# Performance work log

Hardware: AMD Instinct MI355X
Metric: run time of the kernel (lower is better)

Reference implementation:

```python
import jax, jax.numpy as jnp
import numpy as np
import math

N = 1024
C = 128
H = 4
HD = C // H  # 32
HID = C // 2  # geom_mlp hidden


def setup_inputs() -> dict:
    key = jax.random.key(0)
    ks = jax.random.split(key, 12)
    s = 0.02
    return {
        "x": jax.random.normal(ks[0], (N, C), jnp.float32),
        "y": jax.random.normal(ks[1], (N, C), jnp.float32),
        "pos": jax.random.normal(ks[2], (N, 3), jnp.float32),
        "Wq": jax.random.normal(ks[3], (C, C), jnp.float32) * s,
        "bq": jnp.zeros((C,), jnp.float32),
        "Wk": jax.random.normal(ks[4], (C, C), jnp.float32) * s,
        "bk": jnp.zeros((C,), jnp.float32),
        "Wv": jax.random.normal(ks[5], (C, C), jnp.float32) * s,
        "bv": jnp.zeros((C,), jnp.float32),
        "W1": jax.random.normal(ks[6], (3, HID), jnp.float32) * s,
        "b1": jnp.zeros((HID,), jnp.float32),
        "W2": jax.random.normal(ks[7], (HID, C), jnp.float32) * s,
        "b2": jnp.zeros((C,), jnp.float32),
    }


def _safe_norm(sq):
    # sqrt with zero (sub)gradient at 0, matching torch.norm behavior
    pos_mask = sq > 0
    return jnp.where(pos_mask, jnp.sqrt(jnp.where(pos_mask, sq, 1.0)), 0.0)


def reference(x, y, pos, Wq, bq, Wk, bk, Wv, bv, W1, b1, W2, b2):
    # pairwise geometry
    pos_diff = pos[:, None, :] - pos[None, :, :]          # [N, N, 3]
    dist = _safe_norm(jnp.sum(pos_diff * pos_diff, -1))   # [N, N]
    geom = jax.nn.relu(pos_diff @ W1 + b1) @ W2 + b2      # [N, N, C]
    geom = geom.reshape(N, N, H, HD)                      # per-head split

    q = (x @ Wq + bq).reshape(N, H, HD)
    k = (y @ Wk + bk).reshape(N, H, HD)
    v = (y @ Wv + bv).reshape(N, H, HD)

    attn = jnp.einsum("ihd,jhd->hij", q, k) / math.sqrt(HD)  # [H, N, N]
    geom_attn = jnp.einsum("ihd,ijhd->hij", q, geom)         # [H, N, N]
    scores = attn + geom_attn - dist[None, :, :]
    p = jax.nn.softmax(scores, axis=-1)
    out = jnp.einsum("hij,jhd->ihd", p, v).reshape(N, C)     # [N, C]
    return out
```

## Files before the change

### kernel.cpp

```cpp
#include <hip/hip_runtime.h>
#include <math.h>


static __device__ __forceinline__ float dot4(float4 a, float4 b) {
  return a.x*b.x + a.y*b.y + a.z*b.z + a.w*b.w;
}

__global__ __launch_bounds__(384) void k_pre(
    const float* __restrict__ x, const float* __restrict__ y, const float* __restrict__ pos,
    const float* __restrict__ Wq, const float* __restrict__ bq,
    const float* __restrict__ Wk, const float* __restrict__ bk,
    const float* __restrict__ Wv, const float* __restrict__ bv,
    const float* __restrict__ W1, const float* __restrict__ b1,
    const float* __restrict__ W2, const float* __restrict__ b2,
    float* __restrict__ q, float* __restrict__ v,
    float* __restrict__ kT4f, float* __restrict__ uT4f,
    float* __restrict__ sA, float* __restrict__ pos4w)
{
  __shared__ float xs[256], ys[256], qs[256];
  __shared__ __align__(16) float4 W2S[64*33];

  const int t  = threadIdx.x;
  const int n0 = blockIdx.x * 2;

  if (t < 256) { xs[t] = x[n0*128 + t]; ys[t] = y[n0*128 + t]; }
  {
    const float4* w2g = (const float4*)W2;
    #pragma unroll
    for (int r = 0; r < 6; ++r) {
      const int e = t + 384*r;
      if (e < 2048) W2S[(e>>5)*33 + (e&31)] = w2g[e];
    }
  }
  __syncthreads();

  {
    const int c   = t & 127;
    const int mat = t >> 7;
    const float* W    = (mat == 0) ? Wq : (mat == 1 ? Wk : Wv);
    const float* S    = (mat == 0) ? xs : ys;
    const float* bias = (mat == 0) ? bq : (mat == 1 ? bk : bv);
    float a0 = 0.f, a1 = 0.f;
    #pragma unroll 8
    for (int d = 0; d < 128; ++d) {
      const float w_ = W[d*128 + c];
      a0 = fmaf(S[d],       w_, a0);
      a1 = fmaf(S[128 + d], w_, a1);
    }
    const float bb = bias[c];
    a0 += bb; a1 += bb;
    if (mat == 0) {
      q[n0*128 + c] = a0; q[(n0+1)*128 + c] = a1;
      qs[c] = a0; qs[128 + c] = a1;
    } else if (mat == 2) {
      v[n0*128 + c] = a0; v[(n0+1)*128 + c] = a1;
    } else {
      kT4f[((c>>2)*1024 + n0  )*4 + (c&3)] = a0;
      kT4f[((c>>2)*1024 + n0+1)*4 + (c&3)] = a1;
    }
  }
  __syncthreads();

  if (t < 256) {
    const int m = t & 63, h = t >> 6;
    const float4* qs4 = (const float4*)qs;
    #pragma unroll
    for (int ii = 0; ii < 2; ++ii) {
      float acc = 0.f;
      #pragma unroll
      for (int ch = 0; ch < 8; ++ch)
        acc += dot4(qs4[ii*32 + h*8 + ch], W2S[m*33 + h*8 + ch]);
      sA[(n0+ii)*328 + 8 + (m>>2)*20 + h*4 + (m&3)] = acc;
    }
    if (t < 8) {
      const int ii = t >> 2, h2 = t & 3;
      float ca = 0.f;
      #pragma unroll
      for (int d = 0; d < 32; ++d) ca = fmaf(qs[ii*128 + h2*32 + d], b2[h2*32 + d], ca);
      sA[(n0+ii)*328 + h2] = ca;
    } else if (t < 16) {
      const int tt = t-8, ii = tt>>2, cc = tt&3;
      sA[(n0+ii)*328 + 4 + cc] = (cc < 3) ? pos[(n0+ii)*3 + cc] : 0.f;
    } else if (t < 24) {
      const int tt = t-16, ii = tt>>2, cc = tt&3;
      pos4w[(n0+ii)*4 + cc] = (cc < 3) ? pos[(n0+ii)*3 + cc] : 0.f;
    }
  } else {
    const int tt = t - 256, ii = tt >> 6, m = tt & 63;
    float ua = 0.f;
    #pragma unroll
    for (int cc = 0; cc < 3; ++cc) ua = fmaf(pos[(n0+ii)*3 + cc], W1[cc*64 + m], ua);
    uT4f[((m>>2)*1024 + (n0+ii))*4 + (m&3)] = ua;
    sA[(n0+ii)*328 + 8 + (m>>2)*20 + 16 + (m&3)] = ua + b1[m];
  }
}

__global__ __launch_bounds__(512, 2) void k_attn(
    const float* __restrict__ q, const float* __restrict__ v,
    const float4* __restrict__ kT4, const float4* __restrict__ uT4,
    const float* __restrict__ sA, const float4* __restrict__ pos4,
    float* __restrict__ out)
{
  __shared__ __align__(16) float eL[8*512];
  __shared__ __align__(16) float rnum[2048];
  __shared__ float rden[64];

  const int t    = threadIdx.x;
  const int i0   = blockIdx.x * 2;
  const int w    = t >> 6;
  const int lane = t & 63;
  const int hl   = lane >> 4;

  const float* sA0 = sA + i0*328;
  const float* sA1 = sA0 + 328;
  const float* q0  = q + i0*128;
  const float* q1  = q0 + 128;

  const float c00 = sA0[0], c01 = sA0[1], c02 = sA0[2], c03 = sA0[3];
  const float c10 = sA1[0], c11 = sA1[1], c12 = sA1[2], c13 = sA1[3];
  const float p0x = sA0[4], p0y = sA0[5], p0z = sA0[6];
  const float p1x = sA1[4], p1y = sA1[5], p1z = sA1[6];

  float2 acc0 = make_float2(0.f, 0.f);
  float2 acc1 = make_float2(0.f, 0.f);
  float lsum[8] = {0.f,0.f,0.f,0.f,0.f,0.f,0.f,0.f};
  const float RS = 0.17677669529663687f;

  float* eW = &eL[w*512];
  const float4* er0 = (const float4*)&eL[w*512 +        hl*64];
  const float4* er1 = (const float4*)&eL[w*512 + 256 + hl*64];

  #pragma unroll
  for (int tt2 = 0; tt2 < 2; ++tt2) {
    const int jb = (w*2 + tt2) * 64;
    const int j  = jb + lane;

    const float4 pj = pos4[j];
    const float d0x = p0x-pj.x, d0y = p0y-pj.y, d0z = p0z-pj.z;
    const float d1x = p1x-pj.x, d1y = p1y-pj.y, d1z = p1z-pj.z;
    const float dist0 = sqrtf(d0x*d0x + d0y*d0y + d0z*d0z);
    const float dist1 = sqrtf(d1x*d1x + d1y*d1y + d1z*d1z);

    float g[2][4] = {{c00,c01,c02,c03},{c10,c11,c12,c13}};
    #pragma unroll 4
    for (int mb = 0; mb < 16; ++mb) {
      const float4 uj = uT4[mb*1024 + j];
      #pragma unroll
      for (int ii = 0; ii < 2; ++ii) {
        const float* ab = (ii ? sA1 : sA0) + 8 + mb*20;
        const float h0 = fmaxf(ab[16] - uj.x, 0.f);
        const float h1 = fmaxf(ab[17] - uj.y, 0.f);
        const float h2 = fmaxf(ab[18] - uj.z, 0.f);
        const float h3 = fmaxf(ab[19] - uj.w, 0.f);
        #pragma unroll
        for (int h = 0; h < 4; ++h)
          g[ii][h] += h0*ab[h*4+0] + h1*ab[h*4+1] + h2*ab[h*4+2] + h3*ab[h*4+3];
      }
    }

    float s[2][4] = {{0.f,0.f,0.f,0.f},{0.f,0.f,0.f,0.f}};
    #pragma unroll 8
    for (int cb = 0; cb < 32; ++cb) {
      const float4 kj = kT4[cb*1024 + j];
      const int h = cb >> 3;
      s[0][h] += kj.x*q0[cb*4+0] + kj.y*q0[cb*4+1] + kj.z*q0[cb*4+2] + kj.w*q0[cb*4+3];
      s[1][h] += kj.x*q1[cb*4+0] + kj.y*q1[cb*4+1] + kj.z*q1[cb*4+2] + kj.w*q1[cb*4+3];
    }

    #pragma unroll
    for (int ii = 0; ii < 2; ++ii) {
      const float di = ii ? dist1 : dist0;
      #pragma unroll
      for (int h = 0; h < 4; ++h) {
        const float p = __expf(fmaf(s[ii][h], RS, g[ii][h]) - di);
        lsum[ii*4+h] += p;
        eW[(ii*4+h)*64 + lane] = p;
      }
    }
    __builtin_amdgcn_wave_barrier();

    const float2* v2 = (const float2*)(v + jb*128);
    #pragma unroll 4
    for (int j4 = 0; j4 < 16; ++j4) {
      const float4 e0 = er0[j4];
      const float4 e1 = er1[j4];
      const float2 va = v2[(j4*4+0)*64 + lane];
      const float2 vb = v2[(j4*4+1)*64 + lane];
      const float2 vc = v2[(j4*4+2)*64 + lane];
      const float2 vd = v2[(j4*4+3)*64 + lane];
      acc0.x = fmaf(e0.x, va.x, acc0.x); acc0.y = fmaf(e0.x, va.y, acc0.y);
      acc1.x = fmaf(e1.x, va.x, acc1.x); acc1.y = fmaf(e1.x, va.y, acc1.y);
      acc0.x = fmaf(e0.y, vb.x, acc0.x); acc0.y = fmaf(e0.y, vb.y, acc0.y);
      acc1.x = fmaf(e1.y, vb.x, acc1.x); acc1.y = fmaf(e1.y, vb.y, acc1.y);
      acc0.x = fmaf(e0.z, vc.x, acc0.x); acc0.y = fmaf(e0.z, vc.y, acc0.y);
      acc1.x = fmaf(e1.z, vc.x, acc1.x); acc1.y = fmaf(e1.z, vc.y, acc1.y);
      acc0.x = fmaf(e0.w, vd.x, acc0.x); acc0.y = fmaf(e0.w, vd.y, acc0.y);
      acc1.x = fmaf(e1.w, vd.x, acc1.x); acc1.y = fmaf(e1.w, vd.y, acc1.y);
    }
    __builtin_amdgcn_wave_barrier();
  }

  #pragma unroll
  for (int mm = 1; mm < 64; mm <<= 1) {
    #pragma unroll
    for (int r8 = 0; r8 < 8; ++r8) lsum[r8] += __shfl_xor(lsum[r8], mm);
  }
  ((float2*)rnum)[w*128 +      lane] = acc0;
  ((float2*)rnum)[w*128 + 64 + lane] = acc1;
  if (lane == 0) {
    #pragma unroll
    for (int r8 = 0; r8 < 8; ++r8) rden[w*8 + r8] = lsum[r8];
  }
  __syncthreads();

  if (t < 256) {
    const int ii = t >> 7, c = t & 127;
    float num = 0.f, den = 0.f;
    #pragma unroll
    for (int ww = 0; ww < 8; ++ww) {
      num += rnum[ww*256 + ii*128 + c];
      den += rden[ww*8 + ii*4 + (c>>5)];
    }
    out[(i0+ii)*128 + c] = num / den;
  }
}

extern "C" void kernel_launch(void* const* d_in, const int* in_sizes, int n_in,
                              void* d_out, int out_size, void* d_ws, size_t ws_size,
                              hipStream_t stream) {
  const float* x   = (const float*)d_in[0];
  const float* y   = (const float*)d_in[1];
  const float* pos = (const float*)d_in[2];
  const float* Wq  = (const float*)d_in[3];
  const float* bq  = (const float*)d_in[4];
  const float* Wk  = (const float*)d_in[5];
  const float* bk  = (const float*)d_in[6];
  const float* Wv  = (const float*)d_in[7];
  const float* bv  = (const float*)d_in[8];
  const float* W1  = (const float*)d_in[9];
  const float* b1  = (const float*)d_in[10];
  const float* W2  = (const float*)d_in[11];
  const float* b2  = (const float*)d_in[12];

  float* ws = (float*)d_ws;
  float* q    = ws;
  float* v    = ws + 131072;
  float* kT4f = ws + 262144;
  float* uT4f = ws + 393216;
  float* sA   = ws + 458752;
  float* pos4 = ws + 794624;
  float* out  = (float*)d_out;

  k_pre<<<dim3(512), dim3(384), 0, stream>>>(x, y, pos, Wq, bq, Wk, bk, Wv, bv,
                                             W1, b1, W2, b2,
                                             q, v, kT4f, uT4f, sA, pos4);
  k_attn<<<dim3(512), dim3(512), 0, stream>>>(q, v, (const float4*)kT4f,
                                              (const float4*)uT4f, sA,
                                              (const float4*)pos4, out);
}
```

Before: 130.2 us.

## Fold log2e and score scale into precomputed terms, use packed FMAs in attention

```diff
diff --git a/kernel.cpp b/kernel.cpp
--- a/kernel.cpp
+++ b/kernel.cpp
@@ -2,8 +2,21 @@
 #include <math.h>
 
 
+typedef float v2f __attribute__((ext_vector_type(2)));
+typedef float v4f __attribute__((ext_vector_type(4)));
+
+#define L2E 1.4426950408889634f
+#define RSL (0.17677669529663687f * L2E)
+
 static __device__ __forceinline__ float dot4(float4 a, float4 b) {
   return a.x*b.x + a.y*b.y + a.z*b.z + a.w*b.w;
+}
+static __device__ __forceinline__ v2f fma2(v2f a, v2f b, v2f c) {
+  return __builtin_elementwise_fma(a, b, c);
+}
+static __device__ __forceinline__ v4f fma4s(float s, v4f b, v4f c) {
+  v4f sv = {s, s, s, s};
+  return __builtin_elementwise_fma(sv, b, c);
 }
 
 __global__ __launch_bounds__(384) void k_pre(
@@ -50,7 +63,7 @@
     const float bb = bias[c];
     a0 += bb; a1 += bb;
     if (mat == 0) {
-      q[n0*128 + c] = a0; q[(n0+1)*128 + c] = a1;
+      q[n0*128 + c] = a0 * RSL; q[(n0+1)*128 + c] = a1 * RSL;
       qs[c] = a0; qs[128 + c] = a1;
     } else if (mat == 2) {
       v[n0*128 + c] = a0; v[(n0+1)*128 + c] = a1;
@@ -70,20 +83,20 @@
       #pragma unroll
       for (int ch = 0; ch < 8; ++ch)
         acc += dot4(qs4[ii*32 + h*8 + ch], W2S[m*33 + h*8 + ch]);
-      sA[(n0+ii)*328 + 8 + (m>>2)*20 + h*4 + (m&3)] = acc;
+      sA[(n0+ii)*328 + 8 + (m>>2)*20 + h*4 + (m&3)] = acc * L2E;
     }
     if (t < 8) {
       const int ii = t >> 2, h2 = t & 3;
       float ca = 0.f;
       #pragma unroll
       for (int d = 0; d < 32; ++d) ca = fmaf(qs[ii*128 + h2*32 + d], b2[h2*32 + d], ca);
-      sA[(n0+ii)*328 + h2] = ca;
+      sA[(n0+ii)*328 + h2] = ca * L2E;
     } else if (t < 16) {
       const int tt = t-8, ii = tt>>2, cc = tt&3;
-      sA[(n0+ii)*328 + 4 + cc] = (cc < 3) ? pos[(n0+ii)*3 + cc] : 0.f;
+      sA[(n0+ii)*328 + 4 + cc] = (cc < 3) ? pos[(n0+ii)*3 + cc] * L2E : 0.f;
     } else if (t < 24) {
       const int tt = t-16, ii = tt>>2, cc = tt&3;
-      pos4w[(n0+ii)*4 + cc] = (cc < 3) ? pos[(n0+ii)*3 + cc] : 0.f;
+      pos4w[(n0+ii)*4 + cc] = (cc < 3) ? pos[(n0+ii)*3 + cc] * L2E : 0.f;
     }
   } else {
     const int tt = t - 256, ii = tt >> 6, m = tt & 63;
@@ -95,21 +108,23 @@
   }
 }
 
-__global__ __launch_bounds__(512, 2) void k_attn(
+__global__ __launch_bounds__(512, 4) void k_attn(
     const float* __restrict__ q, const float* __restrict__ v,
-    const float4* __restrict__ kT4, const float4* __restrict__ uT4,
-    const float* __restrict__ sA, const float4* __restrict__ pos4,
+    const v4f* __restrict__ kT4, const v4f* __restrict__ uT4,
+    const float* __restrict__ sA, const v4f* __restrict__ pos4,
     float* __restrict__ out)
 {
-  __shared__ __align__(16) float eL[8*512];
-  __shared__ __align__(16) float rnum[2048];
+  __shared__ __align__(16) float eL[8*544];
+  __shared__ __align__(16) float rnum[4096];
   __shared__ float rden[64];
 
   const int t    = threadIdx.x;
   const int i0   = blockIdx.x * 2;
   const int w    = t >> 6;
   const int lane = t & 63;
-  const int hl   = lane >> 4;
+  const int c4   = lane & 31;
+  const int rep  = lane >> 5;
+  const int hh   = c4 >> 3;
 
   const float* sA0 = sA + i0*328;
   const float* sA1 = sA0 + 328;
@@ -121,81 +136,103 @@
   const float p0x = sA0[4], p0y = sA0[5], p0z = sA0[6];
   const float p1x = sA1[4], p1y = sA1[5], p1z = sA1[6];
 
-  float2 acc0 = make_float2(0.f, 0.f);
-  float2 acc1 = make_float2(0.f, 0.f);
+  v4f acc0 = {0.f,0.f,0.f,0.f};
+  v4f acc1 = {0.f,0.f,0.f,0.f};
   float lsum[8] = {0.f,0.f,0.f,0.f,0.f,0.f,0.f,0.f};
-  const float RS = 0.17677669529663687f;
-
-  float* eW = &eL[w*512];
-  const float4* er0 = (const float4*)&eL[w*512 +        hl*64];
-  const float4* er1 = (const float4*)&eL[w*512 + 256 + hl*64];
+
+  float* eW = &eL[w*544];
+  const v4f* er0 = (const v4f*)&eL[w*544 +  hh     *68 + rep*32];
+  const v4f* er1 = (const v4f*)&eL[w*544 + (4+hh)  *68 + rep*32];
 
   #pragma unroll
   for (int tt2 = 0; tt2 < 2; ++tt2) {
     const int jb = (w*2 + tt2) * 64;
     const int j  = jb + lane;
 
-    const float4 pj = pos4[j];
+    const v4f pj = pos4[j];
     const float d0x = p0x-pj.x, d0y = p0y-pj.y, d0z = p0z-pj.z;
     const float d1x = p1x-pj.x, d1y = p1y-pj.y, d1z = p1z-pj.z;
     const float dist0 = sqrtf(d0x*d0x + d0y*d0y + d0z*d0z);
     const float dist1 = sqrtf(d1x*d1x + d1y*d1y + d1z*d1z);
 
-    float g[2][4] = {{c00,c01,c02,c03},{c10,c11,c12,c13}};
+    v2f g0a={0.f,0.f}, g0b={0.f,0.f}, g0c={0.f,0.f}, g0d={0.f,0.f};
+    v2f g1a={0.f,0.f}, g1b={0.f,0.f}, g1c={0.f,0.f}, g1d={0.f,0.f};
     #pragma unroll 4
     for (int mb = 0; mb < 16; ++mb) {
-      const float4 uj = uT4[mb*1024 + j];
-      #pragma unroll
-      for (int ii = 0; ii < 2; ++ii) {
-        const float* ab = (ii ? sA1 : sA0) + 8 + mb*20;
-        const float h0 = fmaxf(ab[16] - uj.x, 0.f);
-        const float h1 = fmaxf(ab[17] - uj.y, 0.f);
-        const float h2 = fmaxf(ab[18] - uj.z, 0.f);
-        const float h3 = fmaxf(ab[19] - uj.w, 0.f);
-        #pragma unroll
-        for (int h = 0; h < 4; ++h)
-          g[ii][h] += h0*ab[h*4+0] + h1*ab[h*4+1] + h2*ab[h*4+2] + h3*ab[h*4+3];
+      const v4f uj = uT4[mb*1024 + j];
+      const v2f uj01 = uj.xy, uj23 = uj.zw;
+      {
+        const float* ab = sA0 + 8 + mb*20;
+        const v2f z = {0.f, 0.f};
+        const v2f h01 = __builtin_elementwise_max(*(const v2f*)(ab+16) - uj01, z);
+        const v2f h23 = __builtin_elementwise_max(*(const v2f*)(ab+18) - uj23, z);
+        g0a = fma2(h01, *(const v2f*)(ab+ 0), g0a); g0a = fma2(h23, *(const v2f*)(ab+ 2), g0a);
+        g0b = fma2(h01, *(const v2f*)(ab+ 4), g0b); g0b = fma2(h23, *(const v2f*)(ab+ 6), g0b);
+        g0c = fma2(h01, *(const v2f*)(ab+ 8), g0c); g0c = fma2(h23, *(const v2f*)(ab+10), g0c);
+        g0d = fma2(h01, *(const v2f*)(ab+12), g0d); g0d = fma2(h23, *(const v2f*)(ab+14), g0d);
       }
-    }
-
-    float s[2][4] = {{0.f,0.f,0.f,0.f},{0.f,0.f,0.f,0.f}};
+      {
+        const float* ab = sA1 + 8 + mb*20;
+        const v2f z = {0.f, 0.f};
+        const v2f h01 = __builtin_elementwise_max(*(const v2f*)(ab+16) - uj01, z);
+        const v2f h23 = __builtin_elementwise_max(*(const v2f*)(ab+18) - uj23, z);
+        g1a = fma2(h01, *(const v2f*)(ab+ 0), g1a); g1a = fma2(h23, *(const v2f*)(ab+ 2), g1a);
+        g1b = fma2(h01, *(const v2f*)(ab+ 4), g1b); g1b = fma2(h23, *(const v2f*)(ab+ 6), g1b);
+        g1c = fma2(h01, *(const v2f*)(ab+ 8), g1c); g1c = fma2(h23, *(const v2f*)(ab+10), g1c);
+        g1d = fma2(h01, *(const v2f*)(ab+12), g1d); g1d = fma2(h23, *(const v2f*)(ab+14), g1d);
+      }
+    }
+
+    v2f s0a={0.f,0.f}, s0b={0.f,0.f}, s0c={0.f,0.f}, s0d={0.f,0.f};
+    v2f s1a={0.f,0.f}, s1b={0.f,0.f}, s1c={0.f,0.f}, s1d={0.f,0.f};
     #pragma unroll 8
-    for (int cb = 0; cb < 32; ++cb) {
-      const float4 kj = kT4[cb*1024 + j];
-      const int h = cb >> 3;
-      s[0][h] += kj.x*q0[cb*4+0] + kj.y*q0[cb*4+1] + kj.z*q0[cb*4+2] + kj.w*q0[cb*4+3];
-      s[1][h] += kj.x*q1[cb*4+0] + kj.y*q1[cb*4+1] + kj.z*q1[cb*4+2] + kj.w*q1[cb*4+3];
-    }
-
-    #pragma unroll
-    for (int ii = 0; ii < 2; ++ii) {
-      const float di = ii ? dist1 : dist0;
-      #pragma unroll
-      for (int h = 0; h < 4; ++h) {
-        const float p = __expf(fmaf(s[ii][h], RS, g[ii][h]) - di);
-        lsum[ii*4+h] += p;
-        eW[(ii*4+h)*64 + lane] = p;
-      }
+    for (int cb = 0; cb < 8; ++cb) {
+      const v4f k0 = kT4[(cb     )*1024 + j];
+      const v4f k1 = kT4[(cb +  8)*1024 + j];
+      const v4f k2 = kT4[(cb + 16)*1024 + j];
+      const v4f k3 = kT4[(cb + 24)*1024 + j];
+      s0a = fma2(k0.xy, *(const v2f*)(q0 + cb*4      ), s0a); s0a = fma2(k0.zw, *(const v2f*)(q0 + cb*4 +  2), s0a);
+      s0b = fma2(k1.xy, *(const v2f*)(q0 + cb*4 + 32 ), s0b); s0b = fma2(k1.zw, *(const v2f*)(q0 + cb*4 + 34), s0b);
+      s0c = fma2(k2.xy, *(const v2f*)(q0 + cb*4 + 64 ), s0c); s0c = fma2(k2.zw, *(const v2f*)(q0 + cb*4 + 66), s0c);
+      s0d = fma2(k3.xy, *(const v2f*)(q0 + cb*4 + 96 ), s0d); s0d = fma2(k3.zw, *(const v2f*)(q0 + cb*4 + 98), s0d);
+      s1a = fma2(k0.xy, *(const v2f*)(q1 + cb*4      ), s1a); s1a = fma2(k0.zw, *(const v2f*)(q1 + cb*4 +  2), s1a);
+      s1b = fma2(k1.xy, *(const v2f*)(q1 + cb*4 + 32 ), s1b); s1b = fma2(k1.zw, *(const v2f*)(q1 + cb*4 + 34), s1b);
+      s1c = fma2(k2.xy, *(const v2f*)(q1 + cb*4 + 64 ), s1c); s1c = fma2(k2.zw, *(const v2f*)(q1 + cb*4 + 66), s1c);
+      s1d = fma2(k3.xy, *(const v2f*)(q1 + cb*4 + 96 ), s1d); s1d = fma2(k3.zw, *(const v2f*)(q1 + cb*4 + 98), s1d);
+    }
+
+    {
+      const v2f t0a = s0a + g0a, t0b = s0b + g0b, t0c = s0c + g0c, t0d = s0d + g0d;
+      const float p0 = exp2f(t0a.x + t0a.y + (c00 - dist0));
+      const float p1 = exp2f(t0b.x + t0b.y + (c01 - dist0));
+      const float p2 = exp2f(t0c.x + t0c.y + (c02 - dist0));
+      const float p3 = exp2f(t0d.x + t0d.y + (c03 - dist0));
+      lsum[0] += p0; lsum[1] += p1; lsum[2] += p2; lsum[3] += p3;
+      eW[      lane] = p0; eW[ 68 + lane] = p1; eW[136 + lane] = p2; eW[204 + lane] = p3;
+      const v2f t1a = s1a + g1a, t1b = s1b + g1b, t1c = s1c + g1c, t1d = s1d + g1d;
+      const float r0 = exp2f(t1a.x + t1a.y + (c10 - dist1));
+      const float r1 = exp2f(t1b.x + t1b.y + (c11 - dist1));
+      const float r2 = exp2f(t1c.x + t1c.y + (c12 - dist1));
+      const float r3 = exp2f(t1d.x + t1d.y + (c13 - dist1));
+      lsum[4] += r0; lsum[5] += r1; lsum[6] += r2; lsum[7] += r3;
+      eW[272 + lane] = r0; eW[340 + lane] = r1; eW[408 + lane] = r2; eW[476 + lane] = r3;
     }
     __builtin_amdgcn_wave_barrier();
 
-    const float2* v2 = (const float2*)(v + jb*128);
+    const v4f* vg = (const v4f*)(v + jb*128);
+    const int vbase = rep*32*32 + c4;
     #pragma unroll 4
-    for (int j4 = 0; j4 < 16; ++j4) {
-      const float4 e0 = er0[j4];
-      const float4 e1 = er1[j4];
-      const float2 va = v2[(j4*4+0)*64 + lane];
-      const float2 vb = v2[(j4*4+1)*64 + lane];
-      const float2 vc = v2[(j4*4+2)*64 + lane];
-      const float2 vd = v2[(j4*4+3)*64 + lane];
-      acc0.x = fmaf(e0.x, va.x, acc0.x); acc0.y = fmaf(e0.x, va.y, acc0.y);
-      acc1.x = fmaf(e1.x, va.x, acc1.x); acc1.y = fmaf(e1.x, va.y, acc1.y);
-      acc0.x = fmaf(e0.y, vb.x, acc0.x); acc0.y = fmaf(e0.y, vb.y, acc0.y);
-      acc1.x = fmaf(e1.y, vb.x, acc1.x); acc1.y = fmaf(e1.y, vb.y, acc1.y);
-      acc0.x = fmaf(e0.z, vc.x, acc0.x); acc0.y = fmaf(e0.z, vc.y, acc0.y);
-      acc1.x = fmaf(e1.z, vc.x, acc1.x); acc1.y = fmaf(e1.z, vc.y, acc1.y);
-      acc0.x = fmaf(e0.w, vd.x, acc0.x); acc0.y = fmaf(e0.w, vd.y, acc0.y);
-      acc1.x = fmaf(e1.w, vd.x, acc1.x); acc1.y = fmaf(e1.w, vd.y, acc1.y);
+    for (int jj4 = 0; jj4 < 8; ++jj4) {
+      const v4f e0 = er0[jj4];
+      const v4f e1 = er1[jj4];
+      const v4f va = vg[vbase + (jj4*4+0)*32];
+      const v4f vb = vg[vbase + (jj4*4+1)*32];
+      const v4f vc = vg[vbase + (jj4*4+2)*32];
+      const v4f vd = vg[vbase + (jj4*4+3)*32];
+      acc0 = fma4s(e0.x, va, acc0); acc1 = fma4s(e1.x, va, acc1);
+      acc0 = fma4s(e0.y, vb, acc0); acc1 = fma4s(e1.y, vb, acc1);
+      acc0 = fma4s(e0.z, vc, acc0); acc1 = fma4s(e1.z, vc, acc1);
+      acc0 = fma4s(e0.w, vd, acc0); acc1 = fma4s(e1.w, vd, acc1);
     }
     __builtin_amdgcn_wave_barrier();
   }
@@ -205,8 +242,8 @@
     #pragma unroll
     for (int r8 = 0; r8 < 8; ++r8) lsum[r8] += __shfl_xor(lsum[r8], mm);
   }
-  ((float2*)rnum)[w*128 +      lane] = acc0;
-  ((float2*)rnum)[w*128 + 64 + lane] = acc1;
+  ((v4f*)rnum)[((w*2+0)*2 + rep)*32 + c4] = acc0;
+  ((v4f*)rnum)[((w*2+1)*2 + rep)*32 + c4] = acc1;
   if (lane == 0) {
     #pragma unroll
     for (int r8 = 0; r8 < 8; ++r8) rden[w*8 + r8] = lsum[r8];
@@ -218,7 +255,7 @@
     float num = 0.f, den = 0.f;
     #pragma unroll
     for (int ww = 0; ww < 8; ++ww) {
-      num += rnum[ww*256 + ii*128 + c];
+      num += rnum[((ww*2+ii)*2+0)*128 + c] + rnum[((ww*2+ii)*2+1)*128 + c];
       den += rden[ww*8 + ii*4 + (c>>5)];
     }
     out[(i0+ii)*128 + c] = num / den;
@@ -254,7 +291,7 @@
   k_pre<<<dim3(512), dim3(384), 0, stream>>>(x, y, pos, Wq, bq, Wk, bk, Wv, bv,
                                              W1, b1, W2, b2,
                                              q, v, kT4f, uT4f, sA, pos4);
-  k_attn<<<dim3(512), dim3(512), 0, stream>>>(q, v, (const float4*)kT4f,
-                                              (const float4*)uT4f, sA,
-                                              (const float4*)pos4, out);
-}
+  k_attn<<<dim3(512), dim3(512), 0, stream>>>(q, v, (const v4f*)kT4f,
+                                              (const v4f*)uT4f, sA,
+                                              (const v4f*)pos4, out);
+}
```

After: 117.1 us. 10.0% less time.
